# Kernel optimization log

Measured on AMD Instinct MI355X. Metric: run time of the kernel, lower is better.

Reference implementation:

```python
import jax, jax.numpy as jnp
import numpy as np

B_IN, B_L1, B_L2 = 64, 16, 8
F1, F2, F_OUT = 64, 128, 10
BATCH = 16
CPLX = jnp.complex64

# ---------- numpy precompute: quadrature weights, Wigner-d matrices, grids ----------

def _dh_weights(b):
    # Driscoll-Healy quadrature weights over the 2b beta samples
    j = np.arange(2 * b)
    l = np.arange(b)
    s = np.sin(np.outer(2 * j + 1, 2 * l + 1) * np.pi / (4 * b)) @ (1.0 / (2 * l + 1))
    return ((2.0 / b) * np.sin(np.pi * (2 * j + 1) / (4 * b)) * s).astype(np.float32)

def _wigner_d_all(lmax, betas):
    # d^l(beta) = exp(-i beta Jy) via eigendecomposition of Jy (quantum convention)
    betas = np.asarray(betas, np.float64)
    out = []
    for l in range(lmax + 1):
        m = np.arange(-l, l)
        cp = np.sqrt(l * (l + 1) - m * (m + 1))
        Jy = np.zeros((2 * l + 1, 2 * l + 1), np.complex128)
        Jy[np.arange(1, 2 * l + 1), np.arange(0, 2 * l)] = -0.5j * cp
        Jy[np.arange(0, 2 * l), np.arange(1, 2 * l + 1)] = 0.5j * cp
        lam, V = np.linalg.eigh(Jy)
        ph = np.exp(-1j * np.outer(betas, lam))
        d = np.einsum('mk,bk,nk->bmn', V, ph, V.conj())
        out.append(np.ascontiguousarray(d.real.astype(np.float32)))
    return out

def _s2_grid():
    beta = np.arange(1, 4) * (np.pi / 8) / 3
    alpha = np.linspace(0, 2 * np.pi, 8, endpoint=False)
    B, A = np.meshgrid(beta, alpha, indexing='ij')
    return B.ravel(), A.ravel()

def _so3_grid():
    beta = np.arange(1, 4) * (np.pi / 8) / 3
    alpha = np.linspace(0, 2 * np.pi, 8, endpoint=False)
    pre_gamma = np.linspace(0, 2 * np.pi, 8, endpoint=False)
    B, A, C = np.meshgrid(beta, alpha, pre_gamma, indexing='ij')
    return B.ravel(), A.ravel(), (C - A).ravel()

_BETAS_IN = np.pi * (2 * np.arange(2 * B_IN) + 1) / (4 * B_IN)
_BETAS_L1 = np.pi * (2 * np.arange(2 * B_L1) + 1) / (4 * B_L1)
_BETAS_L2 = np.pi * (2 * np.arange(2 * B_L2) + 1) / (4 * B_L2)
_W_IN = jnp.asarray(_dh_weights(B_IN))
_W_L1 = jnp.asarray(_dh_weights(B_L1))
_W_L2 = jnp.asarray(_dh_weights(B_L2))
_D_IN = _wigner_d_all(B_L1 - 1, _BETAS_IN)
_D_L1 = _wigner_d_all(B_L1 - 1, _BETAS_L1)
_D_L2 = _wigner_d_all(B_L2 - 1, _BETAS_L2)
_GB2, _GA2 = _s2_grid()
_GB3, _GA3, _GC3 = _so3_grid()
_D_G2 = _wigner_d_all(B_L1 - 1, _GB2)
_D_G3 = _wigner_d_all(B_L2 - 1, _GB3)

# spherical-harmonic / Wigner-D basis evaluated at kernel grid points
_PSI_S2 = []
for l in range(B_L1):
    m = np.arange(-l, l + 1)
    _PSI_S2.append(jnp.asarray((_D_G2[l][:, :, l].T * np.exp(-1j * np.outer(m, _GA2))).astype(np.complex64)))
_PSI_SO3 = []
for l in range(B_L2):
    m = np.arange(-l, l + 1)
    em = np.exp(-1j * np.outer(m, _GA3))
    en = np.exp(-1j * np.outer(m, _GC3))
    _PSI_SO3.append(jnp.asarray((_D_G3[l].transpose(1, 2, 0) * em[:, None, :] * en[None, :, :]).astype(np.complex64)))
_DCOL_IN = [jnp.asarray(_D_IN[l][:, :, l]) for l in range(B_L1)]  # d^l_{m,0}(beta_k)
_D_L1_J = [jnp.asarray(d) for d in _D_L1]
_D_L2_J = [jnp.asarray(d) for d in _D_L2]

# ---------- jax forward ----------

def _s2_fft(x):
    # x: [batch, f, 2b_in, 2b_in] (beta, alpha) -> list over l of [2l+1, batch, f] complex
    n = 2 * B_IN
    xf = jnp.fft.fft(x.astype(CPLX), axis=-1)  # e^{-i m alpha}
    out = []
    for l in range(B_L1):
        mi = np.arange(-l, l + 1) % n
        Xl = xf[..., mi]  # [batch, f, 2b, 2l+1]
        out.append(jnp.einsum('k,km,bfkm->mbf', _W_IN, _DCOL_IN[l], Xl) * (2 * np.pi / n))
    return out

def _so3_ifft(Fz, d_list, b):
    # Fz: list over l of [2l+1, 2l+1, batch, f] -> real [batch, f, 2b, 2b, 2b] (beta,alpha,gamma)
    n = 2 * b
    batch, f = Fz[0].shape[2], Fz[0].shape[3]
    S = jnp.zeros((batch, f, n, n, n), CPLX)
    for l in range(b):
        mi = np.arange(-l, l + 1) % n
        C = (2 * l + 1) * jnp.einsum('kmn,mnbf->bfkmn', d_list[l].astype(CPLX), Fz[l])
        S = S.at[:, :, :, mi[:, None], mi[None, :]].add(C)
    return jnp.real(jnp.fft.ifft2(S, axes=(-2, -1))) * (n * n)  # e^{+i m alpha} e^{+i n gamma}

def _so3_fft(x, d_list, w, b_l):
    # x: [batch, f, 2b, 2b, 2b] real -> list over l<b_l of [2l+1, 2l+1, batch, f] complex
    n = x.shape[-1]
    xf = jnp.fft.fft2(x.astype(CPLX), axes=(-2, -1)) / (n * n)
    out = []
    for l in range(b_l):
        mi = np.arange(-l, l + 1) % n
        Xl = xf[:, :, :, mi[:, None], mi[None, :]]  # [batch, f, 2b, 2l+1, 2l+1]
        out.append(jnp.einsum('k,kmn,bfkmn->mnbf', w, d_list[l], Xl) * (2 * np.pi))
    return out

def _forward(x, w1, w2, lin_w, lin_b):
    # S2Convolution: spectral x spectral-kernel outer product per degree l
    Fx = _s2_fft(x)
    Fy = [jnp.einsum('iog,mg->mio', w1.astype(CPLX), p) for p in _PSI_S2]
    Fz = [jnp.einsum('mbi,nio->mnbo', Fx[l], jnp.conj(Fy[l])) for l in range(B_L1)]
    y1 = jax.nn.relu(_so3_ifft(Fz, _D_L1_J, B_L1))
    # SO3Convolution
    Fx2 = _so3_fft(y1, _D_L1_J, _W_L1, B_L2)
    Fy2 = [jnp.einsum('iog,mng->mnio', w2.astype(CPLX), p) for p in _PSI_SO3]
    Fz2 = [jnp.einsum('mkbi,nkio->mnbo', Fx2[l], jnp.conj(Fy2[l])) for l in range(B_L2)]
    y2 = jax.nn.relu(_so3_ifft(Fz2, _D_L2_J, B_L2))
    # so3_integrate: quadrature over beta, uniform mean over alpha,gamma
    feat = jnp.einsum('k,bfk->bf', _W_L2, y2.mean(axis=(-2, -1)))
    return feat @ lin_w.T + lin_b


def setup_inputs() -> dict:
    key = jax.random.key(0)
    k1, k2, k3, k4 = jax.random.split(key, 4)
    x = jax.random.normal(k1, (BATCH, 1, 2 * B_IN, 2 * B_IN), jnp.float32)
    w1 = jax.random.normal(k2, (1, F1, 24), jnp.float32) / np.float32(np.sqrt(24))
    w2 = jax.random.normal(k3, (F1, F2, 192), jnp.float32) / np.float32(np.sqrt(192 * F1))
    lin_w = jax.random.normal(k4, (F_OUT, F2), jnp.float32) / np.float32(np.sqrt(F2))
    lin_b = jnp.zeros((F_OUT,), jnp.float32)
    return {'x': x, 'w1': w1, 'w2': w2, 'lin_w': lin_w, 'lin_b': lin_b}


def reference(x, w1, w2, lin_w, lin_b):
    return _forward(x, w1, w2, lin_w, lin_b)
```

## Files before the change

kernel.cpp:

```cpp
#include <hip/hip_runtime.h>
#include <cmath>
#include <vector>
#include <algorithm>

enum : int {
  OFF_WIN  = 0,
  OFF_WL1  = 128,
  OFF_WL2  = 160,
  OFF_DCOL = 176,
  OFF_D1A  = OFF_DCOL + 32768,
  OFF_D1B  = OFF_D1A + 174592,
  OFF_D2   = OFF_D1B + 174592,
  OFF_PSI2 = OFF_D2 + 10880,
  OFF_PSI3 = OFF_PSI2 + 12288,
  CONST_TOTAL = OFF_PSI3 + 261120
};

static constexpr size_t OFS_XF1  = 0;
static constexpr size_t OFS_FX   = 507904;
static constexpr size_t OFS_FY1  = 540672;
static constexpr size_t OFS_FX2  = 671744;
static constexpr size_t OFS_FY2  = 6242304;
static constexpr size_t OFS_FZ2  = 50806784;
static constexpr size_t OFS_W2T  = OFS_FZ2;
static constexpr size_t OFS_FEAT = 61947904;
static constexpr size_t WS_NEEDED = 61956096;

static inline int off3h(int l){ return (4*l*l*l - l)/3; }

namespace {

double fact_[32];
void init_fact(){ fact_[0]=1.0; for(int i=1;i<32;i++) fact_[i]=fact_[i-1]*i; }

void wigner_d(int l, double beta, double* d){
  int n = 2*l+1;
  double cb = std::cos(beta*0.5), sb = std::sin(beta*0.5);
  for(int r=0;r<n;r++){ int mp = r-l;
    for(int c=0;c<n;c++){ int m = c-l;
      double f = std::sqrt(fact_[l+mp]*fact_[l-mp]*fact_[l+m]*fact_[l-m]);
      int s0 = std::max(0, m-mp), s1 = std::min(l+m, l-mp);
      double sum = 0;
      for(int s=s0;s<=s1;s++){
        double t = (((mp-m+s)&1)? -1.0 : 1.0)
                 / (fact_[l+m-s]*fact_[s]*fact_[mp-m+s]*fact_[l-mp-s]);
        t *= std::pow(cb, (double)(2*l+m-mp-2*s)) * std::pow(sb, (double)(mp-m+2*s));
        sum += t;
      }
      d[r*n+c] = f*sum;
    }
  }
}

void dh_weights(int b, double* w){
  for(int j=0;j<2*b;j++){
    double s = 0;
    for(int l=0;l<b;l++) s += std::sin((2.0*j+1)*(2.0*l+1)*M_PI/(4.0*b))/(2.0*l+1);
    w[j] = (2.0/b)*std::sin(M_PI*(2.0*j+1)/(4.0*b))*s;
  }
}

float* g_const = nullptr;

struct ConstInit {
  ConstInit(){
    init_fact();
    std::vector<float> h((size_t)CONST_TOTAL, 0.0f);
    std::vector<double> tmp(31*31);
    std::vector<double> wl1(32);
    { std::vector<double> w(128); dh_weights(64, w.data()); for(int i=0;i<128;i++) h[OFF_WIN+i]=(float)w[i]; }
    { dh_weights(16, wl1.data()); for(int i=0;i<32;i++)  h[OFF_WL1+i]=(float)wl1[i]; }
    { std::vector<double> w(16);  dh_weights(8,  w.data()); for(int i=0;i<16;i++)  h[OFF_WL2+i]=(float)w[i]; }
    for(int l=0;l<16;l++){ int n=2*l+1;
      for(int k=0;k<128;k++){
        wigner_d(l, M_PI*(2.0*k+1)/256.0, tmp.data());
        for(int mi=0;mi<n;mi++) h[OFF_DCOL + (size_t)(l*l+mi)*128 + k] = (float)tmp[mi*n + l];
      }
    }
    for(int l=0;l<16;l++){ int n=2*l+1;
      for(int k=0;k<32;k++){
        wigner_d(l, M_PI*(2.0*k+1)/64.0, tmp.data());
        for(int t=0;t<n*n;t++){
          size_t base = (size_t)(off3h(l)+t)*32 + k;
          h[OFF_D1A + base] = (float)((2*l+1)*tmp[t]);
          if(l < 8)
            h[OFF_D1B + base] = (float)(2.0*M_PI*wl1[k]*tmp[t]/1024.0);
        }
      }
    }
    for(int l=0;l<8;l++){ int n=2*l+1;
      for(int k=0;k<16;k++){
        wigner_d(l, M_PI*(2.0*k+1)/32.0, tmp.data());
        for(int t=0;t<n*n;t++)
          h[OFF_D2 + (size_t)(off3h(l)+t)*16 + k] = (float)((2*l+1)*tmp[t]);
      }
    }
    for(int l=0;l<16;l++){ int n=2*l+1;
      for(int i=0;i<3;i++){
        wigner_d(l, (i+1)*(M_PI/8.0)/3.0, tmp.data());
        for(int j=0;j<8;j++){
          double alpha = 2.0*M_PI*j/8.0;
          int g = i*8+j;
          for(int mi=0;mi<n;mi++){
            double d = tmp[mi*n + l];
            double th = (double)(mi-l)*alpha;
            size_t base = OFF_PSI2 + ((size_t)(l*l+mi)*24 + g)*2;
            h[base+0] = (float)( d*std::cos(th));
            h[base+1] = (float)(-d*std::sin(th));
          }
        }
      }
    }
    for(int l=0;l<8;l++){ int n=2*l+1;
      for(int i=0;i<3;i++){
        wigner_d(l, (i+1)*(M_PI/8.0)/3.0, tmp.data());
        for(int j=0;j<8;j++){
          double alpha = 2.0*M_PI*j/8.0;
          for(int kk=0;kk<8;kk++){
            double gamma = 2.0*M_PI*kk/8.0 - alpha;
            int g = (i*8+j)*8+kk;
            for(int mi=0;mi<n;mi++) for(int ni=0;ni<n;ni++){
              double d = tmp[mi*n+ni];
              double th = (double)(mi-l)*alpha + (double)(ni-l)*gamma;
              size_t base = OFF_PSI3 + (((size_t)off3h(l)+ (size_t)mi*n+ni)*192 + g)*2;
              h[base+0] = (float)( d*std::cos(th));
              h[base+1] = (float)(-d*std::sin(th));
            }
          }
        }
      }
    }
    hipMalloc((void**)&g_const, sizeof(float)*(size_t)CONST_TOTAL);
    hipMemcpy(g_const, h.data(), sizeof(float)*(size_t)CONST_TOTAL, hipMemcpyHostToDevice);
  }
};
ConstInit g_init_;

}

__device__ __forceinline__ int off3d(int l){ return (4*l*l*l - l)/3; }
constexpr float TWO_PI_F = 6.28318530717958647692f;

__device__ __forceinline__ unsigned int f2bf(float f){
  union { float f; unsigned int u; } v; v.f = f;
  unsigned int r = v.u + 0x7FFFu + ((v.u >> 16) & 1u);
  return r >> 16;
}
__device__ __forceinline__ unsigned int pk2(float2 v){
  return f2bf(v.x) | (f2bf(v.y) << 16);
}
__device__ __forceinline__ float bflo(unsigned int u){
  union { unsigned int u; float f; } c; c.u = u << 16; return c.f;
}
__device__ __forceinline__ float bfhi(unsigned int u){
  union { unsigned int u; float f; } c; c.u = u & 0xffff0000u; return c.f;
}

typedef __attribute__((ext_vector_type(8))) short bf16x8;
typedef __attribute__((ext_vector_type(4))) float f32x4;

__global__ void k_fft_alpha(const float* __restrict__ x, float2* __restrict__ xf1){
  __shared__ float row[128];
  __shared__ float2 w128[128];
  __shared__ float2 red2[4][31];
  int r = blockIdx.x;
  int t = threadIdx.x;
  row[t] = x[(size_t)r*128 + t];
  float ang = (TWO_PI_F/128.0f)*t;
  w128[t] = make_float2(cosf(ang), sinf(ang));
  __syncthreads();
  int mi = t & 31, part = t >> 5;
  if(mi < 31){
    int m = mi - 15;
    float2 acc = make_float2(0.f,0.f);
    int a0 = part*32;
    for(int a=a0;a<a0+32;a++){
      float2 w = w128[(m*a)&127];
      acc.x += row[a]*w.x;
      acc.y -= row[a]*w.y;
    }
    red2[part][mi] = acc;
  }
  __syncthreads();
  if(t < 31){
    float2 s = red2[0][t];
    float2 s1 = red2[1][t], s2 = red2[2][t], s3 = red2[3][t];
    s.x += s1.x + s2.x + s3.x;
    s.y += s1.y + s2.y + s3.y;
    xf1[(size_t)r*31 + t] = s;
  }
}

__global__ void k_fx(const float* __restrict__ cst, const float2* __restrict__ xf1,
                     float2* __restrict__ FxP){
  __shared__ float2 redL[256];
  int lp = threadIdx.x & 63;
  int kc = threadIdx.x >> 6;
  int idx = blockIdx.x*64 + lp;
  int c2 = idx >> 4, b = idx & 15;
  int l = 0; while((l+1)*(l+1) <= c2) l++;
  int m = (c2 - l*l) - l;
  const float* W  = cst + OFF_WIN;
  const float* DC = cst + OFF_DCOL + (size_t)c2*128;
  float2 acc = make_float2(0.f,0.f);
  int k0 = kc*32;
  for(int k=k0;k<k0+32;k++){
    float wv = W[k]*DC[k];
    float2 xv = xf1[((size_t)b*128+k)*31 + (m+15)];
    acc.x += wv*xv.x; acc.y += wv*xv.y;
  }
  redL[threadIdx.x] = acc;
  __syncthreads();
  if(kc == 0){
    float2 p1 = redL[lp+64], p2 = redL[lp+128], p3 = redL[lp+192];
    acc.x += p1.x + p2.x + p3.x;
    acc.y += p1.y + p2.y + p3.y;
    float s = TWO_PI_F/128.0f;
    FxP[(size_t)c2*16+b] = make_float2(acc.x*s, acc.y*s);
  }
}

__global__ void k_fy1(const float* __restrict__ cst, const float* __restrict__ w1,
                      float2* __restrict__ FyP){
  int idx = blockIdx.x*blockDim.x + threadIdx.x;
  int c2 = idx >> 6, o = idx & 63;
  const float2* psi = (const float2*)(cst + OFF_PSI2) + (size_t)c2*24;
  const float* w1r = w1 + (size_t)o*24;
  float2 acc = make_float2(0.f,0.f);
  for(int g=0;g<24;g++){
    float wv = w1r[g];
    float2 p = psi[g];
    acc.x += wv*p.x; acc.y += wv*p.y;
  }
  FyP[(size_t)c2*64+o] = acc;
}

__global__ void __launch_bounds__(256,4) k_conv1(const float* __restrict__ cst,
                                                 const float2* __restrict__ FxP,
                                                 const float2* __restrict__ FyP,
                                                 unsigned int* __restrict__ FxB){
  __shared__ __align__(16) char L[39936];
  float2* FxL = (float2*)L;
  float2* FyL = FxL + 256;
  float2* SB  = (float2*)(L + 4096);
  unsigned int* yBu = (unsigned int*)(L + 4096);
  float2* XfB = (float2*)(L + 4096);
  unsigned int* TBu = (unsigned int*)(L + 23936);
  float2* T2B = (float2*)(L + 23936);
  float2* acc2= (float2*)(L + 34176);
  float2* w32 = (float2*)(L + 39616);
  int*    o3T = (int*)(L + 39872);

  int b = blockIdx.x >> 6, o = blockIdx.x & 63;
  int tid = threadIdx.x;
  if(tid < 32){ float ang = (TWO_PI_F/32.0f)*tid; w32[tid] = make_float2(cosf(ang), sinf(ang)); }
  if(tid < 16){ int l = tid; o3T[l] = (4*l*l*l - l)/3; }
  FxL[tid] = FxP[(size_t)tid*16 + b];
  FyL[tid] = FyP[(size_t)tid*64 + o];
  for(int t=tid; t<680; t+=256) acc2[t] = make_float2(0.f,0.f);

  const float* D1A = cst + OFF_D1A;
  const float* D1B = cst + OFF_D1B;

  for(int kt=0; kt<8; kt++){
    int k0 = kt*4;
    __syncthreads();
    for(int t=tid; t<496; t+=256){
      int mi = t/31, niq = t - mi*31;
      int n = niq-15;
      int an = n<0?-n:n;
      int lmin = mi>an?mi:an;
      float2 s0={0,0},s1={0,0},s2={0,0},s3={0,0};
      for(int l=lmin;l<16;l++){
        int c = 2*l+1, l2 = l*l;
        float2 fx = FxL[l2+l+mi];
        float2 fy = FyL[l2+(n+l)];
        float zx = fx.x*fy.x + fx.y*fy.y;
        float zy = fx.y*fy.x - fx.x*fy.y;
        const float4* dp = (const float4*)(D1A + (((size_t)o3T[l] + (mi+l)*c + (n+l))<<5) + k0);
        float4 d0 = dp[0];
        s0.x += d0.x*zx; s0.y += d0.x*zy;
        s1.x += d0.y*zx; s1.y += d0.y*zy;
        s2.x += d0.z*zx; s2.y += d0.z*zy;
        s3.x += d0.w*zx; s3.y += d0.w*zy;
      }
      float2* sp = SB + (size_t)t*5;
      sp[0]=s0; sp[1]=s1; sp[2]=s2; sp[3]=s3;
    }
    __syncthreads();
    {
      int mi = tid >> 4, cp = tid & 15;
      float2 a0[4], a1[4];
      #pragma unroll
      for(int j=0;j<4;j++){ a0[j]=make_float2(0,0); a1[j]=make_float2(0,0); }
      float2 step = w32[cp];
      float2 wv = w32[(15*cp)&31];
      float2 cur = make_float2(wv.x, -wv.y);
      const float2* srow = SB + (size_t)(mi*31)*5;
      for(int nb=0; nb<31; nb++){
        float2 q0 = srow[nb*5+0], q1 = srow[nb*5+1], q2 = srow[nb*5+2], q3 = srow[nb*5+3];
        float px, py;
        bool odd = (nb & 1);
        #define K1STEP(QX,QY,J) \
          px = QX*cur.x - QY*cur.y; py = QX*cur.y + QY*cur.x; \
          a0[J].x += px; a0[J].y += py; \
          if(odd){ a1[J].x += px; a1[J].y += py; } else { a1[J].x -= px; a1[J].y -= py; }
        K1STEP(q0.x,q0.y,0) K1STEP(q1.x,q1.y,1)
        K1STEP(q2.x,q2.y,2) K1STEP(q3.x,q3.y,3)
        #undef K1STEP
        float nx = cur.x*step.x - cur.y*step.y;
        cur.y = cur.x*step.y + cur.y*step.x;
        cur.x = nx;
      }
      unsigned int* tp0 = TBu + (size_t)(mi*32+cp)*5;
      tp0[0]=pk2(a0[0]); tp0[1]=pk2(a0[1]); tp0[2]=pk2(a0[2]); tp0[3]=pk2(a0[3]);
      unsigned int* tp1 = TBu + (size_t)(mi*32+cp+16)*5;
      tp1[0]=pk2(a1[0]); tp1[1]=pk2(a1[1]); tp1[2]=pk2(a1[2]); tp1[3]=pk2(a1[3]);
    }
    __syncthreads();
    {
      int c = tid & 31, aq = tid >> 5;
      float y0[4],y1[4],y2[4],y3[4], t0x[4];
      {
        const unsigned int* t0p = TBu + (size_t)c*5;
        t0x[0]=bflo(t0p[0]); t0x[1]=bflo(t0p[1]); t0x[2]=bflo(t0p[2]); t0x[3]=bflo(t0p[3]);
      }
      #pragma unroll
      for(int j=0;j<4;j++){ y0[j]=0; y1[j]=0; y2[j]=0; y3[j]=0; }
      #pragma unroll
      for(int m=1;m<16;m++){
        float2 w = w32[(m*aq)&31];
        const unsigned int* tp = TBu + (size_t)(m*32+c)*5;
        unsigned int d0=tp[0], d1=tp[1], d2=tp[2], d3=tp[3];
        float tx[4] = {bflo(d0),bflo(d1),bflo(d2),bflo(d3)};
        float ty[4] = {bfhi(d0),bfhi(d1),bfhi(d2),bfhi(d3)};
        #pragma unroll
        for(int j=0;j<4;j++){
          float px = tx[j]*w.x - ty[j]*w.y;
          float py = tx[j]*w.y + ty[j]*w.x;
          y0[j] += px;
          int r = m & 3;
          if(r==0){ y1[j] += px; y3[j] += px; }
          else if(r==1){ y1[j] -= py; y3[j] += py; }
          else if(r==2){ y1[j] -= px; y3[j] -= px; }
          else { y1[j] += py; y3[j] -= py; }
          y2[j] += (m&1)? -px : px;
        }
      }
      #define YWRITE(A, YV) { \
        float v0 = t0x[0]+2.f*YV[0], v1 = t0x[1]+2.f*YV[1], v2 = t0x[2]+2.f*YV[2], v3 = t0x[3]+2.f*YV[3]; \
        v0 = v0>0?v0:0; v1 = v1>0?v1:0; v2 = v2>0?v2:0; v3 = v3>0?v3:0; \
        unsigned int* yp = yBu + ((size_t)(A)*32 + c)*3; \
        yp[0] = f2bf(v0) | (f2bf(v1)<<16); \
        yp[1] = f2bf(v2) | (f2bf(v3)<<16); }
      YWRITE(aq,    y0)
      YWRITE(aq+8,  y1)
      YWRITE(aq+16, y2)
      YWRITE(aq+24, y3)
      #undef YWRITE
    }
    __syncthreads();
    {
      int mp = tid >> 5, c4 = tid & 31;
      float2 t2[4];
      #pragma unroll
      for(int j=0;j<4;j++) t2[j]=make_float2(0,0);
      for(int a=0;a<32;a++){
        float2 w = w32[(mp*a)&31];
        const unsigned int* yp = yBu + ((size_t)a*32 + c4)*3;
        unsigned int d0 = yp[0], d1 = yp[1];
        float yv[4] = {bflo(d0), bfhi(d0), bflo(d1), bfhi(d1)};
        #pragma unroll
        for(int j=0;j<4;j++){
          t2[j].x += yv[j]*w.x;
          t2[j].y -= yv[j]*w.y;
        }
      }
      float2* tp = T2B + (size_t)(mp*32+c4)*5;
      tp[0]=t2[0]; tp[1]=t2[1]; tp[2]=t2[2]; tp[3]=t2[3];
    }
    __syncthreads();
    if(tid < 120){
      int mp = tid/15, npq = tid - mp*15;
      int np = npq-7;
      float2 xf[4];
      #pragma unroll
      for(int j=0;j<4;j++) xf[j]=make_float2(0,0);
      float2 wv = w32[np&31];
      float2 step = make_float2(wv.x, -wv.y);
      float2 cur = make_float2(1.f, 0.f);
      const float2* trow = T2B + (size_t)(mp*32)*5;
      for(int c=0;c<32;c++){
        float2 q0 = trow[c*5+0], q1 = trow[c*5+1], q2 = trow[c*5+2], q3 = trow[c*5+3];
        float tx[4] = {q0.x,q1.x,q2.x,q3.x};
        float ty[4] = {q0.y,q1.y,q2.y,q3.y};
        #pragma unroll
        for(int j=0;j<4;j++){
          xf[j].x += tx[j]*cur.x - ty[j]*cur.y;
          xf[j].y += tx[j]*cur.y + ty[j]*cur.x;
        }
        float nx = cur.x*step.x - cur.y*step.y;
        cur.y = cur.x*step.y + cur.y*step.x;
        cur.x = nx;
      }
      float2* xp = XfB + (size_t)tid*5;
      xp[0]=xf[0]; xp[1]=xf[1]; xp[2]=xf[2]; xp[3]=xf[3];
    }
    __syncthreads();
    if(tid < 225){
      int mi2 = tid/15, ni2 = tid - mi2*15;
      int mp = mi2-7, np = ni2-7;
      float2 xf[4];
      if(mp >= 0){
        const float2* xp = XfB + (size_t)(mp*15+ni2)*5;
        xf[0]=xp[0]; xf[1]=xp[1]; xf[2]=xp[2]; xf[3]=xp[3];
      } else {
        const float2* xp = XfB + (size_t)((-mp)*15+(14-ni2))*5;
        float2 q0=xp[0],q1=xp[1],q2=xp[2],q3=xp[3];
        xf[0]=make_float2(q0.x,-q0.y); xf[1]=make_float2(q1.x,-q1.y);
        xf[2]=make_float2(q2.x,-q2.y); xf[3]=make_float2(q3.x,-q3.y);
      }
      int am = mp<0?-mp:mp, an = np<0?-np:np;
      int lmin = am>an?am:an;
      for(int l=lmin;l<8;l++){
        int c2 = 2*l+1;
        int cidx = o3T[l] + (mp+l)*c2 + (np+l);
        const float4* dp = (const float4*)(D1B + (((size_t)cidx)<<5) + k0);
        float4 d0 = dp[0];
        float rx = d0.x*xf[0].x + d0.y*xf[1].x + d0.z*xf[2].x + d0.w*xf[3].x;
        float ry = d0.x*xf[0].y + d0.y*xf[1].y + d0.z*xf[2].y + d0.w*xf[3].y;
        float2 cur = acc2[cidx];
        cur.x += rx; cur.y += ry;
        acc2[cidx] = cur;
      }
    }
  }
  __syncthreads();
  for(int t=tid; t<680; t+=256){
    float2 v = acc2[t];
    unsigned int pk = f2bf(v.x) | (f2bf(v.y) << 16);
    FxB[(size_t)t*1024 + b*64 + o] = pk;
  }
}

__global__ void k_w2t(const float* __restrict__ w2, float* __restrict__ w2t){
  int idx = blockIdx.x*256 + threadIdx.x;
  int g = idx >> 13, q = idx & 8191;
  int i = q & 63, o = q >> 6;
  w2t[idx] = w2[((size_t)i*128 + o)*192 + g];
}

__global__ void __launch_bounds__(256) k_fy2(const float* __restrict__ cst,
                                             const float* __restrict__ w2t,
                                             unsigned int* __restrict__ FyB){
  __shared__ __align__(16) float2 psiL[8*192];
  int cg  = blockIdx.x >> 5;
  int iog = blockIdx.x & 31;
  int tid = threadIdx.x;
  int q   = iog*256 + tid;
  int i   = q & 63, o = q >> 6;
  const float2* psi = (const float2*)(cst + OFF_PSI3) + (size_t)cg*8*192;
  for(int t=tid; t<1536; t+=256) psiL[t] = psi[t];
  __syncthreads();
  float2 acc[8];
  #pragma unroll
  for(int j=0;j<8;j++) acc[j] = make_float2(0.f,0.f);
  const float4* psiL4 = (const float4*)psiL;
  for(int g=0; g<192; g+=2){
    float w0 = w2t[(size_t)g*8192 + q];
    float w1 = w2t[(size_t)(g+1)*8192 + q];
    int gh = g >> 1;
    #pragma unroll
    for(int j=0;j<8;j++){
      float4 p = psiL4[j*96 + gh];
      acc[j].x += w0*p.x + w1*p.z;
      acc[j].y += w0*p.y + w1*p.w;
    }
  }
  #pragma unroll
  for(int j=0;j<8;j++){
    size_t base = (size_t)(cg*8+j)*16384;
    unsigned int r  = f2bf(acc[j].x);
    unsigned int im = f2bf(acc[j].y);
    unsigned int nim= f2bf(-acc[j].y);
    FyB[base + (size_t)(2*o  )*64 + i] = r  | (im << 16);
    FyB[base + (size_t)(2*o+1)*64 + i] = nim| (r  << 16);
  }
}

__global__ void __launch_bounds__(256) k_fz2(const unsigned int* __restrict__ FxB,
                                             const unsigned int* __restrict__ FyB,
                                             float* __restrict__ Fz2f){
  int p = blockIdx.x >> 1, nb = blockIdx.x & 1;
  int c, o3, q;
  if(p < 113)      { c=15; o3=455; q=p; }
  else if(p < 198) { c=13; o3=286; q=p-113; }
  else if(p < 259) { c=11; o3=165; q=p-198; }
  else if(p < 300) { c=9;  o3=84;  q=p-259; }
  else if(p < 325) { c=7;  o3=35;  q=p-300; }
  else if(p < 338) { c=5;  o3=10;  q=p-325; }
  else if(p < 343) { c=3;  o3=1;   q=p-338; }
  else             { c=1;  o3=0;   q=0; }
  int mi = q / c, ni = q - mi*c;
  int lh = c >> 1;

  int tid  = threadIdx.x;
  int lane = tid & 63, wv = tid >> 6;
  int m16  = lane & 15, quad = lane >> 4;

  int nrow = nb*128 + wv*32 + m16;
  int aoff = m16*128 + quad*8;
  int boff = nrow*128 + quad*8;

  f32x4 acc0 = {0,0,0,0}, acc1 = {0,0,0,0};

  const unsigned short* FxS = (const unsigned short*)FxB;
  const unsigned short* FyS = (const unsigned short*)FyB;

  for(int kk=0; kk<c; kk++){
    const unsigned short* Arow = FxS + (size_t)(o3 + mi*c + kk)*2048;
    const unsigned short* Brow = FyS + (size_t)(o3 + ni*c + kk)*32768;
    #pragma unroll
    for(int ig=0; ig<4; ig++){
      bf16x8 af = *(const bf16x8*)(Arow + aoff + ig*32);
      bf16x8 b0 = *(const bf16x8*)(Brow + boff          + ig*32);
      bf16x8 b1 = *(const bf16x8*)(Brow + boff + 2048   + ig*32);
      acc0 = __builtin_amdgcn_mfma_f32_16x16x32_bf16(af, b0, acc0, 0,0,0);
      acc1 = __builtin_amdgcn_mfma_f32_16x16x32_bf16(af, b1, acc1, 0,0,0);
    }
  }
  int coefC = o3 + mi*c + ni;
  float* dst = Fz2f + (size_t)coefC*4096;
  int npb = nrow;
  #pragma unroll
  for(int r=0;r<4;r++){
    int b = quad*4 + r;
    dst[(size_t)b*256 + npb     ] = acc0[r];
    dst[(size_t)b*256 + npb + 16] = acc1[r];
  }
  if(!(mi==lh && ni==lh)){
    int coefM = o3 + (c-1-mi)*c + (c-1-ni);
    float sg = (((mi+ni) + (npb&1)) & 1) ? -1.f : 1.f;
    float* dst2 = Fz2f + (size_t)coefM*4096;
    #pragma unroll
    for(int r=0;r<4;r++){
      int b = quad*4 + r;
      dst2[(size_t)b*256 + npb     ] = sg*acc0[r];
      dst2[(size_t)b*256 + npb + 16] = sg*acc1[r];
    }
  }
}

__global__ void __launch_bounds__(256) k_slice2(const float* __restrict__ cst,
                                                const float2* __restrict__ Fz2P,
                                                float* __restrict__ featP){
  __shared__ float2 FzL[680];
  __shared__ float2 S2[225];
  __shared__ float2 TA[240];
  __shared__ float2 w16[16];
  __shared__ float red[256];
  int bo = blockIdx.x;
  int tid = threadIdx.x;
  if(tid < 16){ float ang = (TWO_PI_F/16.0f)*tid; w16[tid] = make_float2(cosf(ang), sinf(ang)); }
  for(int t=tid; t<680; t+=256) FzL[t] = Fz2P[(size_t)t*2048 + bo];
  __syncthreads();
  const float* D2  = cst + OFF_D2;
  const float* WL2 = cst + OFF_WL2;
  float part = 0.f;
  for(int k2=0;k2<16;k2++){
    if(tid < 225){
      int mi = tid/15, ni = tid%15;
      int m = mi-7, n = ni-7;
      int am = m<0?-m:m, an = n<0?-n:n;
      int lmin = am>an?am:an;
      float2 acc = make_float2(0.f,0.f);
      for(int l=lmin;l<8;l++){
        int c = 2*l+1;
        int idx = off3d(l) + (m+l)*c + (n+l);
        float dv = D2[((size_t)idx<<4) + k2];
        float2 fzv = FzL[idx];
        acc.x += dv*fzv.x; acc.y += dv*fzv.y;
      }
      S2[tid] = acc;
    }
    __syncthreads();
    if(tid < 240){
      int mi = tid >> 4, c = tid & 15;
      float2 acc = make_float2(0.f,0.f);
      for(int ni=0;ni<15;ni++){
        float2 sv = S2[mi*15+ni];
        float2 w = w16[((ni-7)*c)&15];
        acc.x += sv.x*w.x - sv.y*w.y;
        acc.y += sv.x*w.y + sv.y*w.x;
      }
      TA[mi*16+c] = acc;
    }
    __syncthreads();
    {
      int a = tid >> 4, c = tid & 15;
      float acc = 0.f;
      for(int mi=0;mi<15;mi++){
        float2 tv = TA[mi*16+c];
        float2 w = w16[((mi-7)*a)&15];
        acc += tv.x*w.x - tv.y*w.y;
      }
      if(acc > 0.f) part += WL2[k2]*acc;
    }
    __syncthreads();
  }
  red[tid] = part;
  __syncthreads();
  for(int s=128;s>0;s>>=1){ if(tid<s) red[tid]+=red[tid+s]; __syncthreads(); }
  if(tid==0) featP[bo] = red[0]*(1.0f/256.0f);
}

__global__ void k_out(const float* __restrict__ featP, const float* __restrict__ lin_w,
                      const float* __restrict__ lin_b, float* __restrict__ out){
  int t = threadIdx.x;
  if(t < 160){
    int b = t/10, j = t%10;
    float acc = lin_b[j];
    for(int o=0;o<128;o++) acc += featP[b*128+o]*lin_w[j*128+o];
    out[t] = acc;
  }
}

extern "C" void kernel_launch(void* const* d_in, const int* in_sizes, int n_in,
                              void* d_out, int out_size, void* d_ws, size_t ws_size,
                              hipStream_t stream){
  const float* x     = (const float*)d_in[0];
  const float* w1    = (const float*)d_in[1];
  const float* w2    = (const float*)d_in[2];
  const float* lin_w = (const float*)d_in[3];
  const float* lin_b = (const float*)d_in[4];
  float* out = (float*)d_out;
  if(ws_size < WS_NEEDED) return;
  char* ws = (char*)d_ws;
  float2* xf1  = (float2*)(ws + OFS_XF1);
  float2* FxP  = (float2*)(ws + OFS_FX);
  float2* FyP  = (float2*)(ws + OFS_FY1);
  unsigned int* FxB = (unsigned int*)(ws + OFS_FX2);
  unsigned int* FyB = (unsigned int*)(ws + OFS_FY2);
  float2* Fz2P = (float2*)(ws + OFS_FZ2);
  float*  w2tP = (float*)(ws + OFS_W2T);
  float*  featP= (float*)(ws + OFS_FEAT);
  const float* cst = g_const;

  k_fft_alpha<<<2048, 128, 0, stream>>>(x, xf1);
  k_fx      <<<64,   256, 0, stream>>>(cst, xf1, FxP);
  k_fy1     <<<64,   256, 0, stream>>>(cst, w1, FyP);
  k_conv1   <<<1024, 256, 0, stream>>>(cst, FxP, FyP, FxB);
  k_w2t     <<<6144, 256, 0, stream>>>(w2, w2tP);
  k_fy2     <<<2720, 256, 0, stream>>>(cst, w2tP, FyB);
  k_fz2     <<<688,  256, 0, stream>>>(FxB, FyB, (float*)Fz2P);
  k_slice2  <<<2048, 256, 0, stream>>>(cst, Fz2P, featP);
  k_out     <<<1,    256, 0, stream>>>(featP, lin_w, lin_b, out);
}
```

Baseline: 598.1 us.

## Compute Fy2 filter transform with bf16 MFMA instead of scalar FP32 loops

```diff
diff --git a/kernel.cpp b/kernel.cpp
--- a/kernel.cpp
+++ b/kernel.cpp
@@ -13,7 +13,8 @@
   OFF_D2   = OFF_D1B + 174592,
   OFF_PSI2 = OFF_D2 + 10880,
   OFF_PSI3 = OFF_PSI2 + 12288,
-  CONST_TOTAL = OFF_PSI3 + 261120
+  OFF_PSIB = OFF_PSI3 + 261120,
+  CONST_TOTAL = OFF_PSIB + 132096
 };
 
 static constexpr size_t OFS_XF1  = 0;
@@ -22,7 +23,7 @@
 static constexpr size_t OFS_FX2  = 671744;
 static constexpr size_t OFS_FY2  = 6242304;
 static constexpr size_t OFS_FZ2  = 50806784;
-static constexpr size_t OFS_W2T  = OFS_FZ2;
+static constexpr size_t OFS_W2B  = OFS_FZ2;
 static constexpr size_t OFS_FEAT = 61947904;
 static constexpr size_t WS_NEEDED = 61956096;
 
@@ -129,6 +130,25 @@
           }
         }
       }
+    }
+    {
+      auto hf2bf = [](float f)->unsigned short{
+        union{float f; unsigned int u;} v; v.f=f;
+        unsigned int r = v.u + 0x7FFFu + ((v.u>>16)&1u);
+        return (unsigned short)(r>>16);
+      };
+      unsigned short* pb = (unsigned short*)(h.data() + OFF_PSIB);
+      for(int mt=0; mt<43; mt++)
+       for(int reim=0; reim<2; reim++)
+        for(int ks=0; ks<6; ks++)
+         for(int lane=0; lane<64; lane++)
+          for(int j=0; j<8; j++){
+            int coef = mt*16 + (lane&15);
+            int g = ks*32 + (lane>>4)*8 + j;
+            float v = 0.f;
+            if(coef < 680) v = h[OFF_PSI3 + ((size_t)coef*192+g)*2 + reim];
+            pb[((((size_t)mt*2+reim)*6+ks)*64+lane)*8+j] = hf2bf(v);
+          }
     }
     hipMalloc((void**)&g_const, sizeof(float)*(size_t)CONST_TOTAL);
     hipMemcpy(g_const, h.data(), sizeof(float)*(size_t)CONST_TOTAL, hipMemcpyHostToDevice);
@@ -443,48 +463,52 @@
   }
 }
 
-__global__ void k_w2t(const float* __restrict__ w2, float* __restrict__ w2t){
+__global__ void k_w2b(const float* __restrict__ w2, unsigned int* __restrict__ wB){
   int idx = blockIdx.x*256 + threadIdx.x;
-  int g = idx >> 13, q = idx & 8191;
-  int i = q & 63, o = q >> 6;
-  w2t[idx] = w2[((size_t)i*128 + o)*192 + g];
-}
-
-__global__ void __launch_bounds__(256) k_fy2(const float* __restrict__ cst,
-                                             const float* __restrict__ w2t,
-                                             unsigned int* __restrict__ FyB){
-  __shared__ __align__(16) float2 psiL[8*192];
-  int cg  = blockIdx.x >> 5;
-  int iog = blockIdx.x & 31;
+  int io = idx/96, gp = idx - io*96;
+  int i = io & 63, o = io >> 6;
+  const float* src = w2 + ((size_t)i*128 + o)*192 + gp*2;
+  wB[(size_t)io*96 + gp] = f2bf(src[0]) | (f2bf(src[1]) << 16);
+}
+
+__global__ void __launch_bounds__(256) k_fy2m(const float* __restrict__ cst,
+                                              const unsigned int* __restrict__ wB,
+                                              unsigned int* __restrict__ FyB){
+  int mt = blockIdx.x >> 5;
+  int nb = blockIdx.x & 31;
   int tid = threadIdx.x;
-  int q   = iog*256 + tid;
-  int i   = q & 63, o = q >> 6;
-  const float2* psi = (const float2*)(cst + OFF_PSI3) + (size_t)cg*8*192;
-  for(int t=tid; t<1536; t+=256) psiL[t] = psi[t];
-  __syncthreads();
-  float2 acc[8];
+  int lane = tid & 63, wv = tid >> 6;
+  int m16 = lane & 15, quad = lane >> 4;
+  const unsigned short* PB = (const unsigned short*)(cst + OFF_PSIB);
+  bf16x8 aR[6], aI[6];
   #pragma unroll
-  for(int j=0;j<8;j++) acc[j] = make_float2(0.f,0.f);
-  const float4* psiL4 = (const float4*)psiL;
-  for(int g=0; g<192; g+=2){
-    float w0 = w2t[(size_t)g*8192 + q];
-    float w1 = w2t[(size_t)(g+1)*8192 + q];
-    int gh = g >> 1;
+  for(int ks=0; ks<6; ks++){
+    aR[ks] = *(const bf16x8*)(PB + ((((size_t)mt*2+0)*6+ks)*64+lane)*8);
+    aI[ks] = *(const bf16x8*)(PB + ((((size_t)mt*2+1)*6+ks)*64+lane)*8);
+  }
+  const unsigned short* wS = (const unsigned short*)wB;
+  int ioW = nb*256 + wv*64;
+  #pragma unroll
+  for(int t=0; t<4; t++){
+    int io = ioW + t*16 + m16;
+    const unsigned short* brow = wS + (size_t)io*192 + quad*8;
+    f32x4 Dr = {0,0,0,0}, Di = {0,0,0,0};
     #pragma unroll
-    for(int j=0;j<8;j++){
-      float4 p = psiL4[j*96 + gh];
-      acc[j].x += w0*p.x + w1*p.z;
-      acc[j].y += w0*p.y + w1*p.w;
-    }
-  }
-  #pragma unroll
-  for(int j=0;j<8;j++){
-    size_t base = (size_t)(cg*8+j)*16384;
-    unsigned int r  = f2bf(acc[j].x);
-    unsigned int im = f2bf(acc[j].y);
-    unsigned int nim= f2bf(-acc[j].y);
-    FyB[base + (size_t)(2*o  )*64 + i] = r  | (im << 16);
-    FyB[base + (size_t)(2*o+1)*64 + i] = nim| (r  << 16);
+    for(int ks=0; ks<6; ks++){
+      bf16x8 bf = *(const bf16x8*)(brow + ks*32);
+      Dr = __builtin_amdgcn_mfma_f32_16x16x32_bf16(aR[ks], bf, Dr, 0,0,0);
+      Di = __builtin_amdgcn_mfma_f32_16x16x32_bf16(aI[ks], bf, Di, 0,0,0);
+    }
+    int o = io >> 6, i = io & 63;
+    #pragma unroll
+    for(int r=0; r<4; r++){
+      int coef = mt*16 + quad*4 + r;
+      if(coef < 680){
+        size_t base = (size_t)coef*16384;
+        FyB[base + (size_t)(2*o  )*64 + i] = f2bf(Dr[r]) | (f2bf(Di[r]) << 16);
+        FyB[base + (size_t)(2*o+1)*64 + i] = f2bf(-Di[r]) | (f2bf(Dr[r]) << 16);
+      }
+    }
   }
 }
 
@@ -642,7 +666,7 @@
   unsigned int* FxB = (unsigned int*)(ws + OFS_FX2);
   unsigned int* FyB = (unsigned int*)(ws + OFS_FY2);
   float2* Fz2P = (float2*)(ws + OFS_FZ2);
-  float*  w2tP = (float*)(ws + OFS_W2T);
+  unsigned int* wBP = (unsigned int*)(ws + OFS_W2B);
   float*  featP= (float*)(ws + OFS_FEAT);
   const float* cst = g_const;
 
@@ -650,8 +674,8 @@
   k_fx      <<<64,   256, 0, stream>>>(cst, xf1, FxP);
   k_fy1     <<<64,   256, 0, stream>>>(cst, w1, FyP);
   k_conv1   <<<1024, 256, 0, stream>>>(cst, FxP, FyP, FxB);
-  k_w2t     <<<6144, 256, 0, stream>>>(w2, w2tP);
-  k_fy2     <<<2720, 256, 0, stream>>>(cst, w2tP, FyB);
+  k_w2b     <<<3072, 256, 0, stream>>>(w2, wBP);
+  k_fy2m    <<<1376, 256, 0, stream>>>(cst, wBP, FyB);
   k_fz2     <<<688,  256, 0, stream>>>(FxB, FyB, (float*)Fz2P);
   k_slice2  <<<2048, 256, 0, stream>>>(cst, Fz2P, featP);
   k_out     <<<1,    256, 0, stream>>>(featP, lin_w, lin_b, out);
```

Measured after the change: 529.9 us. -11.4%, faster.
